# Optimization experiments

Measured on AMD Instinct MI355X. Metric: run time of the kernel, lower is better.

Reference implementation:

```python
import jax, jax.numpy as jnp
import numpy as np

N_HEAD = 16
N_KV_HEAD = 4
N_EMBD = 2048
HEAD_DIM = N_EMBD // N_HEAD
RMS_EPS = float(np.finfo(np.float32).eps)  # torch F.rms_norm default eps


def setup_inputs() -> dict:
    key = jax.random.key(0)
    ks = jax.random.split(key, 7)
    B, T = 2, 2048
    s = 0.02
    return {
        "x": jax.random.normal(ks[0], (B, T, N_EMBD), jnp.float32),
        "cos": jax.random.uniform(ks[1], (T, 1, HEAD_DIM), jnp.float32),
        "sin": jax.random.uniform(ks[2], (T, 1, HEAD_DIM), jnp.float32),
        "wq": jax.random.normal(ks[3], (N_HEAD * HEAD_DIM, N_EMBD), jnp.float32) * s,
        "wk": jax.random.normal(ks[4], (N_KV_HEAD * HEAD_DIM, N_EMBD), jnp.float32) * s,
        "wv": jax.random.normal(ks[5], (N_KV_HEAD * HEAD_DIM, N_EMBD), jnp.float32) * s,
        "wproj": jax.random.normal(ks[6], (N_EMBD, N_EMBD), jnp.float32) * s,
    }


def _rotate_half(x):
    h = x.shape[-1] // 2
    return jnp.concatenate([-x[..., h:], x[..., :h]], axis=-1)


def _apply_rope(x, cos, sin):  # x: [B, T, H, D]; cos/sin: [T, 1, D]
    return x * cos + _rotate_half(x) * sin


def _rms_norm(x):
    var = jnp.mean(jnp.square(x), axis=-1, keepdims=True)
    return x * jax.lax.rsqrt(var + RMS_EPS)


def reference(x, cos, sin, wq, wk, wv, wproj):
    B, T, C = x.shape
    group = N_HEAD // N_KV_HEAD
    q = (x @ wq.T).reshape(B, T, N_HEAD, HEAD_DIM)
    k = (x @ wk.T).reshape(B, T, N_KV_HEAD, HEAD_DIM)
    v = (x @ wv.T).reshape(B, T, N_KV_HEAD, HEAD_DIM)
    q = _rms_norm(_apply_rope(q, cos, sin))  # RoPE then QK RMSNorm
    k = _rms_norm(_apply_rope(k, cos, sin))
    # to [B, H, T, D]; expand kv heads for GQA
    q = q.transpose(0, 2, 1, 3)
    k = jnp.repeat(k.transpose(0, 2, 1, 3), group, axis=1)
    v = jnp.repeat(v.transpose(0, 2, 1, 3), group, axis=1)
    scale = 1.0 / jnp.sqrt(jnp.asarray(HEAD_DIM, x.dtype))
    scores = jnp.einsum('bhqd,bhkd->bhqk', q, k) * scale
    causal = jnp.tril(jnp.ones((T, T), bool))
    scores = jnp.where(causal, scores, jnp.asarray(-jnp.inf, scores.dtype))
    attn = jax.nn.softmax(scores, axis=-1)
    y = jnp.einsum('bhqk,bhkd->bhqd', attn, v)
    y = y.transpose(0, 2, 1, 3).reshape(B, T, C)
    return y @ wproj.T
```

## Files before the change

### kernel.cpp

```cpp
#include <hip/hip_runtime.h>
#include <hip/hip_bf16.h>

typedef __hip_bfloat16 bf16;
typedef __attribute__((ext_vector_type(8))) __bf16 bf16x8;
typedef __attribute__((ext_vector_type(4))) float f32x4;

#define MFMA16(a, b, c) __builtin_amdgcn_mfma_f32_16x16x32_bf16((a), (b), (c), 0, 0, 0)

#define BT 4096
#define CE 2048
#define NQKV 3072
#define TSEQ 2048
#define HD 128

#define QSCALE (0.08838834764831845f * 1.4426950408889634f)
#define M2 16.3222f

__device__ __forceinline__ void gld16(const void* g, void* l)
{
    __builtin_amdgcn_global_load_lds(
        (const __attribute__((address_space(1))) void*)g,
        (__attribute__((address_space(3))) void*)l, 16, 0, 0);
}

__global__ void detect_dtype(const unsigned short* __restrict__ x, int* __restrict__ flag)
{
    __shared__ int cnt;
    if (threadIdx.x == 0) cnt = 0;
    __syncthreads();
    unsigned short w = x[2 * threadIdx.x];
    int e = (w >> 7) & 0xFF;
    atomicAdd(&cnt, (e >= 117 && e <= 130) ? 1 : 0);
    __syncthreads();
    if (threadIdx.x == 0) *flag = (cnt < 128) ? 1 : 0;
}

__device__ __forceinline__ void stage8(short* dst, const void* src, size_t eoff, bool f32)
{
    if (f32) {
        const float* s = (const float*)src + eoff;
        float4 f0 = *(const float4*)s;
        float4 f1 = *(const float4*)(s + 4);
        bf16x8 v;
        v[0] = (__bf16)f0.x; v[1] = (__bf16)f0.y; v[2] = (__bf16)f0.z; v[3] = (__bf16)f0.w;
        v[4] = (__bf16)f1.x; v[5] = (__bf16)f1.y; v[6] = (__bf16)f1.z; v[7] = (__bf16)f1.w;
        *(bf16x8*)dst = v;
    } else {
        *(uint4*)dst = *(const uint4*)((const bf16*)src + eoff);
    }
}

__device__ __forceinline__ float ldf(const void* p, int i, bool f32)
{
    return f32 ? ((const float*)p)[i] : __bfloat162float(((const bf16*)p)[i]);
}

__global__ __launch_bounds__(256)
void conv_bf16(const void* __restrict__ src, bf16* __restrict__ dst,
               const int* __restrict__ flagp)
{
    const bool f = *flagp != 0;
    size_t i8 = (size_t)blockIdx.x * 256 + threadIdx.x;
    stage8((short*)(dst + i8 * 8), src, i8 * 8, f);
}

__global__ __launch_bounds__(256)
void gemm_bt(const void* __restrict__ A, const bf16* __restrict__ W,
             void* __restrict__ C, int M, int N, int K, int lda,
             int aGate, int oGate, const int* __restrict__ flagp)
{
    __shared__ short As[128][32];
    __shared__ short Bs[128][32];

    const int f = *flagp;
    const bool aF = aGate && f, oF = oGate && f;

    const int tid   = threadIdx.x;
    const int lane  = tid & 63;
    const int wid   = tid >> 6;
    const int row16 = lane & 15;
    const int quad  = lane >> 4;
    const int wr    = wid >> 1;
    const int wc    = wid & 1;
    const int m0    = blockIdx.y * 128;
    const int n0    = blockIdx.x * 128;

    const int rl4 = wid * 16 + (lane >> 2);
    const int c8  = (lane & 3) * 8;

    f32x4 acc[4][4];
#pragma unroll
    for (int i = 0; i < 4; i++)
#pragma unroll
        for (int j = 0; j < 4; j++)
            acc[i][j] = (f32x4){0.f, 0.f, 0.f, 0.f};

    for (int k0 = 0; k0 < K; k0 += 32) {
#pragma unroll
        for (int i = 0; i < 2; i++) {
            int r = i * 64 + rl4;
            gld16(W + (size_t)(n0 + r) * K + k0 + c8, &Bs[r][c8]);
        }
        if (!aF) {
#pragma unroll
            for (int i = 0; i < 2; i++) {
                int r = i * 64 + rl4;
                gld16((const bf16*)A + (size_t)(m0 + r) * lda + k0 + c8, &As[r][c8]);
            }
        } else {
#pragma unroll
            for (int i = 0; i < 2; i++) {
                int c = i * 256 + tid;
                int row = c >> 2, col = (c & 3) << 3;
                stage8(&As[row][col], A, (size_t)(m0 + row) * lda + k0 + col, true);
            }
        }
        __syncthreads();

        bf16x8 af[4], bfv[4];
#pragma unroll
        for (int mi = 0; mi < 4; mi++)
            af[mi] = *(const bf16x8*)&As[wr * 64 + mi * 16 + row16][quad * 8];
#pragma unroll
        for (int ni = 0; ni < 4; ni++)
            bfv[ni] = *(const bf16x8*)&Bs[wc * 64 + ni * 16 + row16][quad * 8];
#pragma unroll
        for (int mi = 0; mi < 4; mi++)
#pragma unroll
            for (int ni = 0; ni < 4; ni++)
                acc[mi][ni] = MFMA16(af[mi], bfv[ni], acc[mi][ni]);
        __syncthreads();
    }

#pragma unroll
    for (int mi = 0; mi < 4; mi++) {
        int rowb = m0 + wr * 64 + mi * 16 + quad * 4;
#pragma unroll
        for (int ni = 0; ni < 4; ni++) {
            int col = n0 + wc * 64 + ni * 16 + row16;
#pragma unroll
            for (int r = 0; r < 4; r++) {
                size_t idx = (size_t)(rowb + r) * N + col;
                float  v   = acc[mi][ni][r];
                if (oF) ((float*)C)[idx] = v;
                else    ((bf16*)C)[idx]  = __float2bfloat16(v);
            }
        }
    }
}

template<int MI>
__global__ __launch_bounds__(512, 2)
void gemmP(const bf16* __restrict__ A, const bf16* __restrict__ W,
           void* __restrict__ C, int M, int N, int K, int lda,
           int oGate, const int* __restrict__ flagp)
{
    constexpr int BM     = MI * 32;
    constexpr int ABYTES = BM * 128;
    constexpr int AUL    = ABYTES / 8192;

    __shared__ __bf16 As[2][BM][64];
    __shared__ __bf16 Bs[2][256][64];

    const bool oF = oGate && (*flagp != 0);

    const int gx  = gridDim.x;
    const int lin = blockIdx.y * gx + blockIdx.x;
    const int cpx = (gx * gridDim.y) >> 3;
    const int swzid = (lin & 7) * cpx + (lin >> 3);
    const int bx = swzid % gx;
    const int by = swzid / gx;

    const int tid   = threadIdx.x;
    const int lane  = tid & 63;
    const int wid   = tid >> 6;
    const int row16 = lane & 15;
    const int quad  = lane >> 4;
    const int wr    = wid >> 2;
    const int wc    = wid & 3;
    const int m0    = by * BM;
    const int n0    = bx * 256;
    const int NT    = K >> 6;

    const int srow = tid >> 3;
    const int sc8  = ((tid & 7) ^ (srow & 7)) * 8;
    const bf16* Ag = A + (size_t)(m0 + srow) * lda + sc8;
    const bf16* Bg = W + (size_t)(n0 + srow) * K   + sc8;
    char* const AsB = (char*)As;
    char* const BsB = (char*)Bs;
    const int sdst = tid * 16;

    auto stA = [&](int kt, int b) {
#pragma unroll
        for (int u = 0; u < AUL; ++u)
            gld16(Ag + (size_t)(u * 64) * lda + kt * 64,
                  AsB + b * ABYTES + u * 8192 + sdst);
    };
    auto stB = [&](int kt, int b) {
#pragma unroll
        for (int u = 0; u < 4; ++u)
            gld16(Bg + (size_t)(u * 64) * K + kt * 64,
                  BsB + b * 32768 + u * 8192 + sdst);
    };

    const int swz  = ((quad ^ (row16 & 7)) * 16);
    const int swz1 = (((4 + quad) ^ (row16 & 7)) * 16);
    const int aRow = wr * (MI * 16) + row16;
    const int bRow = wc * 64 + row16;

    auto ldA = [&](int b, int mi, int kk) -> bf16x8 {
        return *(const bf16x8*)(AsB + b * ABYTES + (aRow + mi * 16) * 128
                                + (kk ? swz1 : swz));
    };
    auto ldB = [&](int b, int ni, int kk) -> bf16x8 {
        return *(const bf16x8*)(BsB + b * 32768 + (bRow + ni * 16) * 128
                                + (kk ? swz1 : swz));
    };

    f32x4 acc[MI][4];
#pragma unroll
    for (int i = 0; i < MI; i++)
#pragma unroll
        for (int j = 0; j < 4; j++)
            acc[i][j] = (f32x4){0.f, 0.f, 0.f, 0.f};

    stA(0, 0); stB(0, 0);
    asm volatile("s_waitcnt vmcnt(0)" ::: "memory");
    __builtin_amdgcn_s_barrier();
    __builtin_amdgcn_sched_barrier(0);

    for (int t = 0; t < NT; ++t) {
        const int rb = t & 1;
        const int wb = rb ^ 1;

        bf16x8 bfr[4][2];
#pragma unroll
        for (int ni = 0; ni < 4; ni++)
#pragma unroll
            for (int kk = 0; kk < 2; kk++)
                bfr[ni][kk] = ldB(rb, ni, kk);
        bf16x8 a0[2][2];
#pragma unroll
        for (int i = 0; i < 2; i++)
#pragma unroll
            for (int kk = 0; kk < 2; kk++)
                a0[i][kk] = ldA(rb, i, kk);

        if (t + 1 < NT) { stB(t + 1, wb); stA(t + 1, wb); }

        __builtin_amdgcn_s_setprio(1);
#pragma unroll
        for (int kk = 0; kk < 2; kk++)
#pragma unroll
            for (int i = 0; i < 2; i++)
#pragma unroll
                for (int ni = 0; ni < 4; ni++)
                    acc[i][ni] = MFMA16(a0[i][kk], bfr[ni][kk], acc[i][ni]);
        __builtin_amdgcn_s_setprio(0);

#pragma unroll
        for (int p = 1; p < MI / 2; ++p) {
            bf16x8 ap[2][2];
#pragma unroll
            for (int i = 0; i < 2; i++)
#pragma unroll
                for (int kk = 0; kk < 2; kk++)
                    ap[i][kk] = ldA(rb, 2 * p + i, kk);
            __builtin_amdgcn_s_setprio(1);
#pragma unroll
            for (int kk = 0; kk < 2; kk++)
#pragma unroll
                for (int i = 0; i < 2; i++)
#pragma unroll
                    for (int ni = 0; ni < 4; ni++)
                        acc[2 * p + i][ni] =
                            MFMA16(ap[i][kk], bfr[ni][kk], acc[2 * p + i][ni]);
            __builtin_amdgcn_s_setprio(0);
        }

        asm volatile("s_waitcnt vmcnt(0)" ::: "memory");
        __builtin_amdgcn_s_barrier();
        __builtin_amdgcn_sched_barrier(0);
    }

#pragma unroll
    for (int mi = 0; mi < MI; mi++) {
        int rowb = m0 + wr * (MI * 16) + mi * 16 + quad * 4;
#pragma unroll
        for (int ni = 0; ni < 4; ni++) {
            int col = n0 + wc * 64 + ni * 16 + row16;
#pragma unroll
            for (int r = 0; r < 4; r++) {
                size_t idx = (size_t)(rowb + r) * N + col;
                float  v   = acc[mi][ni][r];
                if (oF) ((float*)C)[idx] = v;
                else    ((bf16*)C)[idx]  = __float2bfloat16(v);
            }
        }
    }
}

__global__ __launch_bounds__(256)
void rope_rms(bf16* __restrict__ qkv, const void* __restrict__ cosp,
              const void* __restrict__ sinp, const int* __restrict__ flagp)
{
    const bool f = *flagp != 0;
    const int wg   = blockIdx.x * 4 + (threadIdx.x >> 6);
    const int lane = threadIdx.x & 63;
    const int s    = wg % 20;
    const int m    = wg / 20;
    const int t    = m & (TSEQ - 1);

    const int col = (s < 16) ? s * HD : CE + (s - 16) * HD;
    bf16* p = qkv + (size_t)m * NQKV + col;

    float xlo = __bfloat162float(p[lane]);
    float xhi = __bfloat162float(p[lane + 64]);
    float cl  = ldf(cosp, t * HD + lane, f);
    float sl  = ldf(sinp, t * HD + lane, f);
    float ch  = ldf(cosp, t * HD + 64 + lane, f);
    float sh  = ldf(sinp, t * HD + 64 + lane, f);

    float rlo = xlo * cl - xhi * sl;
    float rhi = xhi * ch + xlo * sh;

    float ss = rlo * rlo + rhi * rhi;
#pragma unroll
    for (int off = 32; off > 0; off >>= 1)
        ss += __shfl_xor(ss, off, 64);
    float inv = rsqrtf(ss * (1.0f / 128.0f) + 1.1920929e-07f);
    if (s < 16) inv *= QSCALE;

    p[lane]      = __float2bfloat16(rlo * inv);
    p[lane + 64] = __float2bfloat16(rhi * inv);
}

__global__ __launch_bounds__(256)
void vtrans(const bf16* __restrict__ qkv, bf16* __restrict__ vt)
{
    __shared__ __bf16 tl[64][136];

    const int tid = threadIdx.x;
    const int bh  = blockIdx.x >> 5;
    const int t0  = (blockIdx.x & 31) * 64;
    const int b   = bh >> 2;
    const int hk  = bh & 3;

    const bf16* src = qkv + ((size_t)(b * TSEQ + t0)) * NQKV + 2560 + hk * HD;
#pragma unroll
    for (int it = 0; it < 4; ++it) {
        int idx  = it * 256 + tid;
        int trow = idx >> 4;
        int dcol = (idx & 15) * 8;
        *(uint4*)&tl[trow][dcol] = *(const uint4*)(src + (size_t)trow * NQKV + dcol);
    }
    __syncthreads();

    bf16* dst = vt + ((size_t)(bh * HD)) * TSEQ + t0;
#pragma unroll
    for (int it = 0; it < 4; ++it) {
        int idx  = it * 256 + tid;
        int drow = idx >> 3;
        int tcol = (idx & 7) * 8;
        bf16x8 v;
#pragma unroll
        for (int j = 0; j < 8; ++j)
            v[j] = tl[tcol + j][drow];
        *(bf16x8*)(dst + (size_t)drow * TSEQ + tcol) = v;
    }
}

__global__ __launch_bounds__(512, 2)
void attn(bf16* __restrict__ qkv, const bf16* __restrict__ vt)
{
    __shared__ __bf16 Ks[2][64][128];
    __shared__ __bf16 Vs[2][128][64];
    __shared__ __bf16 Pl[8][16][64];

    const int tid   = threadIdx.x;
    const int lane  = tid & 63;
    const int wid   = tid >> 6;
    const int row16 = lane & 15;
    const int quad  = lane >> 4;
    const int b   = blockIdx.y >> 2;
    const int hk  = blockIdx.y & 3;
    const int h   = hk * 4 + (wid & 3);
    const int mh  = wid >> 2;
    const int p   = blockIdx.x;

    const bf16* Kp = qkv + ((size_t)(b * TSEQ)) * NQKV + CE + hk * HD;
    const bf16* Vp = vt + ((size_t)(b * 4 + hk) * HD) * TSEQ;

    char* const KsB = (char*)Ks;
    char* const VsB = (char*)Vs;
    char* const PlB = (char*)Pl;

    auto stage = [&](int buf, int k0) {
#pragma unroll
        for (int i = 0; i < 2; i++) {
            int kr = (wid << 3) + i * 4 + (lane >> 4);
            int kc = (lane & 15) ^ (kr & 7);
            gld16(Kp + (size_t)(k0 + kr) * NQKV + kc * 8,
                  KsB + buf * 16384 + ((wid << 3) + i * 4) * 256 + lane * 16);
            int vr = (wid << 4) + i * 8 + (lane >> 3);
            int vc = (lane & 7) ^ (vr & 7);
            gld16(Vp + (size_t)vr * TSEQ + k0 + vc * 8,
                  VsB + buf * 16384 + ((wid << 4) + i * 8) * 128 + lane * 16);
        }
    };

    for (int pass = 0; pass < 2; ++pass) {
        const int xi  = pass ? 63 - p : p;
        const int nkt = (xi >> 1) + 1;
        const int qr0 = xi * 32 + mh * 16;

        const bf16* Q = qkv + ((size_t)(b * TSEQ + qr0)) * NQKV + h * HD;
        bf16x8 aq[4];
#pragma unroll
        for (int ds = 0; ds < 4; ds++)
            aq[ds] = *(const bf16x8*)(Q + (size_t)row16 * NQKV + ds * 32 + quad * 8);

        f32x4 o[8];
#pragma unroll
        for (int dt = 0; dt < 8; dt++) o[dt] = (f32x4){0.f, 0.f, 0.f, 0.f};
        float lsum[4] = {0.f, 0.f, 0.f, 0.f};

        __syncthreads();
        stage(0, 0);
        __syncthreads();

        for (int t = 0; t < nkt; ++t) {
            const int cur = t & 1;
            if (t + 1 < nkt) stage(cur ^ 1, (t + 1) * 64);

            f32x4 s[4];
#pragma unroll
            for (int kg = 0; kg < 4; kg++) s[kg] = (f32x4){0.f, 0.f, 0.f, 0.f};
            __builtin_amdgcn_s_setprio(1);
#pragma unroll
            for (int ds = 0; ds < 4; ds++) {
#pragma unroll
                for (int kg = 0; kg < 4; kg++) {
                    int krow = kg * 16 + row16;
                    int phys = (ds * 4 + quad) ^ (row16 & 7);
                    bf16x8 kf = *(const bf16x8*)(KsB + cur * 16384 + krow * 256 + phys * 16);
                    s[kg] = MFMA16(aq[ds], kf, s[kg]);
                }
            }
            __builtin_amdgcn_s_setprio(0);

            const bool diag = (t == nkt - 1);
            const int  k0   = t * 64;
            const int  r16h = row16 >> 3;
            const int  r16l = (row16 & 7) * 2;
#pragma unroll
            for (int r = 0; r < 4; r++) {
                float pv[4];
                int prow = quad * 4 + r;
                int qrow = qr0 + prow;
#pragma unroll
                for (int kg = 0; kg < 4; kg++) {
                    float e = __builtin_amdgcn_exp2f(s[kg][r] - M2);
                    pv[kg] = (!diag || (k0 + kg * 16 + row16 <= qrow)) ? e : 0.f;
                }
                lsum[r] += (pv[0] + pv[1]) + (pv[2] + pv[3]);
#pragma unroll
                for (int kg = 0; kg < 4; kg++)
                    *(__bf16*)(PlB + wid * 2048 + prow * 128
                               + (((kg * 2 + r16h) ^ (prow & 7)) << 4) + r16l)
                        = (__bf16)pv[kg];
            }
            __asm__ volatile("" ::: "memory");

            __builtin_amdgcn_s_setprio(1);
#pragma unroll
            for (int c = 0; c < 2; c++) {
                bf16x8 pf = *(const bf16x8*)(PlB + wid * 2048 + row16 * 128
                                             + ((((c << 2) + quad) ^ (row16 & 7)) << 4));
#pragma unroll
                for (int dt = 0; dt < 8; dt++) {
                    int vrow = dt * 16 + row16;
                    int phys = (c * 4 + quad) ^ (row16 & 7);
                    bf16x8 vf = *(const bf16x8*)(VsB + cur * 16384 + vrow * 128 + phys * 16);
                    o[dt] = MFMA16(pf, vf, o[dt]);
                }
            }
            __builtin_amdgcn_s_setprio(0);
            __asm__ volatile("" ::: "memory");
            __syncthreads();
        }

#pragma unroll
        for (int r = 0; r < 4; r++) {
            float l = lsum[r];
#pragma unroll
            for (int off = 1; off < 16; off <<= 1)
                l += __shfl_xor(l, off, 64);
            float rl = 1.0f / l;
            int trow = qr0 + quad * 4 + r;
            bf16* dst = qkv + ((size_t)(b * TSEQ + trow)) * NQKV + h * HD;
#pragma unroll
            for (int dt = 0; dt < 8; dt++)
                dst[dt * 16 + row16] = __float2bfloat16(o[dt][r] * rl);
        }
    }
}

extern "C" void kernel_launch(void* const* d_in, const int* in_sizes, int n_in,
                              void* d_out, int out_size, void* d_ws, size_t ws_size,
                              hipStream_t stream)
{
    bf16* qkv   = (bf16*)d_ws;
    bf16* vt    = qkv + (size_t)BT * NQKV;
    bf16* wqkvb = vt + (size_t)2 * 4 * HD * TSEQ;
    int* flagp  = (int*)(wqkvb + (size_t)NQKV * CE);
    bf16* xb    = wqkvb + (size_t)NQKV * CE + 16;

    const size_t need = ((size_t)BT * NQKV + (size_t)2 * 4 * HD * TSEQ
                         + (size_t)NQKV * CE + 16 + (size_t)BT * CE) * sizeof(bf16);
    const bool useXb = ws_size >= need;

    detect_dtype<<<1, 256, 0, stream>>>((const unsigned short*)d_in[0], flagp);

    conv_bf16<<<(2048 * 2048 / 8) / 256, 256, 0, stream>>>(d_in[3], wqkvb, flagp);
    conv_bf16<<<(512 * 2048 / 8) / 256, 256, 0, stream>>>(d_in[4], wqkvb + (size_t)2048 * 2048, flagp);
    conv_bf16<<<(512 * 2048 / 8) / 256, 256, 0, stream>>>(d_in[5], wqkvb + (size_t)2560 * 2048, flagp);

    if (useXb) {
        conv_bf16<<<(BT * CE / 8) / 256, 256, 0, stream>>>(d_in[0], xb, flagp);
        gemmP<8><<<dim3(NQKV / 256, BT / 256), 512, 0, stream>>>(
            xb, wqkvb, qkv, BT, NQKV, CE, CE, 0, flagp);
    } else {
        gemm_bt<<<dim3(NQKV / 128, BT / 128), 256, 0, stream>>>(
            d_in[0], wqkvb, qkv, BT, NQKV, CE, CE, 1, 0, flagp);
    }

    conv_bf16<<<(2048 * 2048 / 8) / 256, 256, 0, stream>>>(d_in[6], wqkvb, flagp);

    vtrans<<<256, 256, 0, stream>>>(qkv, vt);

    rope_rms<<<(BT * 20) / 4, 256, 0, stream>>>(qkv, d_in[1], d_in[2], flagp);

    attn<<<dim3(32, 2 * 4), 512, 0, stream>>>(qkv, vt);

    if (useXb) {
        gemmP<4><<<dim3(CE / 256, BT / 128), 512, 0, stream>>>(
            qkv, wqkvb, d_out, BT, CE, CE, NQKV, 1, flagp);
    } else {
        gemm_bt<<<dim3(CE / 128, BT / 128), 256, 0, stream>>>(
            qkv, wqkvb, d_out, BT, CE, CE, NQKV, 0, 1, flagp);
    }
}
```

Measured before the change: 321.0 us.

## Rework bf16 GEMM into triple-buffered pipeline with split K-phase loads and new tiles

```diff
diff --git a/kernel.cpp b/kernel.cpp
--- a/kernel.cpp
+++ b/kernel.cpp
@@ -149,18 +149,22 @@
     }
 }
 
-template<int MI>
+template<int MI, int NI>
 __global__ __launch_bounds__(512, 2)
-void gemmP(const bf16* __restrict__ A, const bf16* __restrict__ W,
+void gemmQ(const bf16* __restrict__ A, const bf16* __restrict__ W,
            void* __restrict__ C, int M, int N, int K, int lda,
            int oGate, const int* __restrict__ flagp)
 {
-    constexpr int BM     = MI * 32;
-    constexpr int ABYTES = BM * 128;
-    constexpr int AUL    = ABYTES / 8192;
-
-    __shared__ __bf16 As[2][BM][64];
-    __shared__ __bf16 Bs[2][256][64];
+    constexpr int BM    = MI * 32;
+    constexpr int BN    = NI * 64;
+    constexpr int ATILE = BM * 128;
+    constexpr int BTILE = BN * 128;
+    constexpr int AUL   = BM / 64;
+    constexpr int BUL   = BN / 64;
+    constexpr int INFL  = AUL + BUL;
+
+    __shared__ __bf16 As[3][BM][64];
+    __shared__ __bf16 Bs[3][BN][64];
 
     const bool oF = oGate && (*flagp != 0);
 
@@ -179,7 +183,7 @@
     const int wr    = wid >> 2;
     const int wc    = wid & 3;
     const int m0    = by * BM;
-    const int n0    = bx * 256;
+    const int n0    = bx * BN;
     const int NT    = K >> 6;
 
     const int srow = tid >> 3;
@@ -190,105 +194,129 @@
     char* const BsB = (char*)Bs;
     const int sdst = tid * 16;
 
-    auto stA = [&](int kt, int b) {
+    auto stA = [&](int kt, int s) {
 #pragma unroll
         for (int u = 0; u < AUL; ++u)
             gld16(Ag + (size_t)(u * 64) * lda + kt * 64,
-                  AsB + b * ABYTES + u * 8192 + sdst);
+                  AsB + s * ATILE + u * 8192 + sdst);
     };
-    auto stB = [&](int kt, int b) {
-#pragma unroll
-        for (int u = 0; u < 4; ++u)
+    auto stB = [&](int kt, int s) {
+#pragma unroll
+        for (int u = 0; u < BUL; ++u)
             gld16(Bg + (size_t)(u * 64) * K + kt * 64,
-                  BsB + b * 32768 + u * 8192 + sdst);
+                  BsB + s * BTILE + u * 8192 + sdst);
     };
 
     const int swz  = ((quad ^ (row16 & 7)) * 16);
     const int swz1 = (((4 + quad) ^ (row16 & 7)) * 16);
     const int aRow = wr * (MI * 16) + row16;
-    const int bRow = wc * 64 + row16;
-
-    auto ldA = [&](int b, int mi, int kk) -> bf16x8 {
-        return *(const bf16x8*)(AsB + b * ABYTES + (aRow + mi * 16) * 128
+    const int bRow = wc * (NI * 16) + row16;
+
+    auto ldA = [&](int sb, int mi, int kk) -> bf16x8 {
+        return *(const bf16x8*)(AsB + sb + (aRow + mi * 16) * 128
                                 + (kk ? swz1 : swz));
     };
-    auto ldB = [&](int b, int ni, int kk) -> bf16x8 {
-        return *(const bf16x8*)(BsB + b * 32768 + (bRow + ni * 16) * 128
+    auto ldB = [&](int sb, int ni, int kk) -> bf16x8 {
+        return *(const bf16x8*)(BsB + sb + (bRow + ni * 16) * 128
                                 + (kk ? swz1 : swz));
     };
 
-    f32x4 acc[MI][4];
+    f32x4 acc[MI][NI];
 #pragma unroll
     for (int i = 0; i < MI; i++)
 #pragma unroll
-        for (int j = 0; j < 4; j++)
+        for (int j = 0; j < NI; j++)
             acc[i][j] = (f32x4){0.f, 0.f, 0.f, 0.f};
 
     stA(0, 0); stB(0, 0);
-    asm volatile("s_waitcnt vmcnt(0)" ::: "memory");
+    stA(1, 1); stB(1, 1);
+    if constexpr (INFL == 5) asm volatile("s_waitcnt vmcnt(5)" ::: "memory");
+    else                     asm volatile("s_waitcnt vmcnt(6)" ::: "memory");
     __builtin_amdgcn_s_barrier();
     __builtin_amdgcn_sched_barrier(0);
 
+    int rs = 0, ps = 2;
     for (int t = 0; t < NT; ++t) {
-        const int rb = t & 1;
-        const int wb = rb ^ 1;
-
-        bf16x8 bfr[4][2];
-#pragma unroll
-        for (int ni = 0; ni < 4; ni++)
-#pragma unroll
-            for (int kk = 0; kk < 2; kk++)
-                bfr[ni][kk] = ldB(rb, ni, kk);
-        bf16x8 a0[2][2];
+        const bool pf = (t + 2) < NT;
+        const int ra  = rs * ATILE;
+        const int rbo = rs * BTILE;
+
+        bf16x8 bfr[NI], aa[2];
+
+#pragma unroll
+        for (int ni = 0; ni < NI; ni++) bfr[ni] = ldB(rbo, ni, 0);
+        aa[0] = ldA(ra, 0, 0); aa[1] = ldA(ra, 1, 0);
+        if (pf) stA(t + 2, ps);
+        __builtin_amdgcn_s_barrier();
+        asm volatile("s_waitcnt lgkmcnt(0)" ::: "memory");
+        __builtin_amdgcn_s_setprio(1);
 #pragma unroll
         for (int i = 0; i < 2; i++)
 #pragma unroll
-            for (int kk = 0; kk < 2; kk++)
-                a0[i][kk] = ldA(rb, i, kk);
-
-        if (t + 1 < NT) { stB(t + 1, wb); stA(t + 1, wb); }
-
+            for (int ni = 0; ni < NI; ni++)
+                acc[i][ni] = MFMA16(aa[i], bfr[ni], acc[i][ni]);
+        __builtin_amdgcn_s_setprio(0);
+        __builtin_amdgcn_s_barrier();
+        __builtin_amdgcn_sched_barrier(0);
+
+        aa[0] = ldA(ra, 2, 0); aa[1] = ldA(ra, 3, 0);
+        __builtin_amdgcn_s_barrier();
+        asm volatile("s_waitcnt lgkmcnt(0)" ::: "memory");
         __builtin_amdgcn_s_setprio(1);
 #pragma unroll
-        for (int kk = 0; kk < 2; kk++)
-#pragma unroll
-            for (int i = 0; i < 2; i++)
-#pragma unroll
-                for (int ni = 0; ni < 4; ni++)
-                    acc[i][ni] = MFMA16(a0[i][kk], bfr[ni][kk], acc[i][ni]);
+        for (int i = 0; i < 2; i++)
+#pragma unroll
+            for (int ni = 0; ni < NI; ni++)
+                acc[2 + i][ni] = MFMA16(aa[i], bfr[ni], acc[2 + i][ni]);
         __builtin_amdgcn_s_setprio(0);
-
-#pragma unroll
-        for (int p = 1; p < MI / 2; ++p) {
-            bf16x8 ap[2][2];
-#pragma unroll
-            for (int i = 0; i < 2; i++)
-#pragma unroll
-                for (int kk = 0; kk < 2; kk++)
-                    ap[i][kk] = ldA(rb, 2 * p + i, kk);
-            __builtin_amdgcn_s_setprio(1);
-#pragma unroll
-            for (int kk = 0; kk < 2; kk++)
-#pragma unroll
-                for (int i = 0; i < 2; i++)
-#pragma unroll
-                    for (int ni = 0; ni < 4; ni++)
-                        acc[2 * p + i][ni] =
-                            MFMA16(ap[i][kk], bfr[ni][kk], acc[2 * p + i][ni]);
-            __builtin_amdgcn_s_setprio(0);
-        }
-
-        asm volatile("s_waitcnt vmcnt(0)" ::: "memory");
         __builtin_amdgcn_s_barrier();
         __builtin_amdgcn_sched_barrier(0);
+
+#pragma unroll
+        for (int ni = 0; ni < NI; ni++) bfr[ni] = ldB(rbo, ni, 1);
+        aa[0] = ldA(ra, 0, 1); aa[1] = ldA(ra, 1, 1);
+        if (pf) stB(t + 2, ps);
+        __builtin_amdgcn_s_barrier();
+        asm volatile("s_waitcnt lgkmcnt(0)" ::: "memory");
+        __builtin_amdgcn_s_setprio(1);
+#pragma unroll
+        for (int i = 0; i < 2; i++)
+#pragma unroll
+            for (int ni = 0; ni < NI; ni++)
+                acc[i][ni] = MFMA16(aa[i], bfr[ni], acc[i][ni]);
+        __builtin_amdgcn_s_setprio(0);
+        __builtin_amdgcn_s_barrier();
+        __builtin_amdgcn_sched_barrier(0);
+
+        aa[0] = ldA(ra, 2, 1); aa[1] = ldA(ra, 3, 1);
+        if (pf) {
+            if constexpr (INFL == 5) asm volatile("s_waitcnt vmcnt(5)" ::: "memory");
+            else                     asm volatile("s_waitcnt vmcnt(6)" ::: "memory");
+        } else {
+            asm volatile("s_waitcnt vmcnt(0)" ::: "memory");
+        }
+        __builtin_amdgcn_s_barrier();
+        asm volatile("s_waitcnt lgkmcnt(0)" ::: "memory");
+        __builtin_amdgcn_s_setprio(1);
+#pragma unroll
+        for (int i = 0; i < 2; i++)
+#pragma unroll
+            for (int ni = 0; ni < NI; ni++)
+                acc[2 + i][ni] = MFMA16(aa[i], bfr[ni], acc[2 + i][ni]);
+        __builtin_amdgcn_s_setprio(0);
+        __builtin_amdgcn_s_barrier();
+        __builtin_amdgcn_sched_barrier(0);
+
+        rs = (rs == 2) ? 0 : rs + 1;
+        ps = (ps == 2) ? 0 : ps + 1;
     }
 
 #pragma unroll
     for (int mi = 0; mi < MI; mi++) {
         int rowb = m0 + wr * (MI * 16) + mi * 16 + quad * 4;
 #pragma unroll
-        for (int ni = 0; ni < 4; ni++) {
-            int col = n0 + wc * 64 + ni * 16 + row16;
+        for (int ni = 0; ni < NI; ni++) {
+            int col = n0 + wc * (NI * 16) + ni * 16 + row16;
 #pragma unroll
             for (int r = 0; r < 4; r++) {
                 size_t idx = (size_t)(rowb + r) * N + col;
@@ -528,7 +556,7 @@
 
     if (useXb) {
         conv_bf16<<<(BT * CE / 8) / 256, 256, 0, stream>>>(d_in[0], xb, flagp);
-        gemmP<8><<<dim3(NQKV / 256, BT / 256), 512, 0, stream>>>(
+        gemmQ<4, 3><<<dim3(NQKV / 192, BT / 128), 512, 0, stream>>>(
             xb, wqkvb, qkv, BT, NQKV, CE, CE, 0, flagp);
     } else {
         gemm_bt<<<dim3(NQKV / 128, BT / 128), 256, 0, stream>>>(
@@ -544,7 +572,7 @@
     attn<<<dim3(32, 2 * 4), 512, 0, stream>>>(qkv, vt);
 
     if (useXb) {
-        gemmP<4><<<dim3(CE / 256, BT / 128), 512, 0, stream>>>(
+        gemmQ<4, 4><<<dim3(CE / 256, BT / 128), 512, 0, stream>>>(
             qkv, wqkvb, d_out, BT, CE, CE, NQKV, 1, flagp);
     } else {
         gemm_bt<<<dim3(CE / 128, BT / 128), 256, 0, stream>>>(
```

New measurement: 343.6 us. 1.07x slower.

## Split attention KV tile across warps with two heads per warp, reduce via LDS

Applied to the files above, without the earlier changes.

```diff
diff --git a/kernel.cpp b/kernel.cpp
--- a/kernel.cpp
+++ b/kernel.cpp
@@ -373,9 +373,10 @@
 __global__ __launch_bounds__(512, 2)
 void attn(bf16* __restrict__ qkv, const bf16* __restrict__ vt)
 {
-    __shared__ __bf16 Ks[2][64][128];
-    __shared__ __bf16 Vs[2][128][64];
-    __shared__ __bf16 Pl[8][16][64];
+    __shared__ char lds[81920];
+    char* const KsB = lds;
+    char* const VsB = lds + 32768;
+    char* const PlB = lds + 65536;
 
     const int tid   = threadIdx.x;
     const int lane  = tid & 63;
@@ -384,16 +385,14 @@
     const int quad  = lane >> 4;
     const int b   = blockIdx.y >> 2;
     const int hk  = blockIdx.y & 3;
-    const int h   = hk * 4 + (wid & 3);
-    const int mh  = wid >> 2;
+    const int hp  = wid & 1;
+    const int mh  = (wid >> 1) & 1;
+    const int ks  = wid >> 2;
+    const int h0  = hk * 4 + hp * 2;
     const int p   = blockIdx.x;
 
     const bf16* Kp = qkv + ((size_t)(b * TSEQ)) * NQKV + CE + hk * HD;
     const bf16* Vp = vt + ((size_t)(b * 4 + hk) * HD) * TSEQ;
-
-    char* const KsB = (char*)Ks;
-    char* const VsB = (char*)Vs;
-    char* const PlB = (char*)Pl;
 
     auto stage = [&](int buf, int k0) {
 #pragma unroll
@@ -414,16 +413,22 @@
         const int nkt = (xi >> 1) + 1;
         const int qr0 = xi * 32 + mh * 16;
 
-        const bf16* Q = qkv + ((size_t)(b * TSEQ + qr0)) * NQKV + h * HD;
-        bf16x8 aq[4];
-#pragma unroll
-        for (int ds = 0; ds < 4; ds++)
-            aq[ds] = *(const bf16x8*)(Q + (size_t)row16 * NQKV + ds * 32 + quad * 8);
-
-        f32x4 o[8];
-#pragma unroll
-        for (int dt = 0; dt < 8; dt++) o[dt] = (f32x4){0.f, 0.f, 0.f, 0.f};
-        float lsum[4] = {0.f, 0.f, 0.f, 0.f};
+        const bf16* Q = qkv + ((size_t)(b * TSEQ + qr0)) * NQKV + h0 * HD;
+        bf16x8 aq[2][4];
+#pragma unroll
+        for (int h2 = 0; h2 < 2; h2++)
+#pragma unroll
+            for (int ds = 0; ds < 4; ds++)
+                aq[h2][ds] = *(const bf16x8*)(Q + h2 * HD
+                             + (size_t)row16 * NQKV + ds * 32 + quad * 8);
+
+        f32x4 o[2][8];
+#pragma unroll
+        for (int h2 = 0; h2 < 2; h2++)
+#pragma unroll
+            for (int dt = 0; dt < 8; dt++)
+                o[h2][dt] = (f32x4){0.f, 0.f, 0.f, 0.f};
+        f32x4 lsum[2] = {(f32x4){0.f,0.f,0.f,0.f}, (f32x4){0.f,0.f,0.f,0.f}};
 
         __syncthreads();
         stage(0, 0);
@@ -433,75 +438,112 @@
             const int cur = t & 1;
             if (t + 1 < nkt) stage(cur ^ 1, (t + 1) * 64);
 
-            f32x4 s[4];
-#pragma unroll
-            for (int kg = 0; kg < 4; kg++) s[kg] = (f32x4){0.f, 0.f, 0.f, 0.f};
+            f32x4 s[2][2];
+#pragma unroll
+            for (int h2 = 0; h2 < 2; h2++)
+#pragma unroll
+                for (int kgl = 0; kgl < 2; kgl++)
+                    s[h2][kgl] = (f32x4){0.f, 0.f, 0.f, 0.f};
             __builtin_amdgcn_s_setprio(1);
 #pragma unroll
             for (int ds = 0; ds < 4; ds++) {
 #pragma unroll
-                for (int kg = 0; kg < 4; kg++) {
-                    int krow = kg * 16 + row16;
-                    int phys = (ds * 4 + quad) ^ (row16 & 7);
-                    bf16x8 kf = *(const bf16x8*)(KsB + cur * 16384 + krow * 256 + phys * 16);
-                    s[kg] = MFMA16(aq[ds], kf, s[kg]);
+                for (int kgl = 0; kgl < 2; kgl++) {
+                    int krow = (ks * 2 + kgl) * 16 + row16;
+                    int phys = (ds * 4 + quad) ^ (krow & 7);
+                    bf16x8 kf = *(const bf16x8*)(KsB + cur * 16384
+                                                 + krow * 256 + phys * 16);
+                    s[0][kgl] = MFMA16(aq[0][ds], kf, s[0][kgl]);
+                    s[1][kgl] = MFMA16(aq[1][ds], kf, s[1][kgl]);
                 }
             }
             __builtin_amdgcn_s_setprio(0);
 
             const bool diag = (t == nkt - 1);
-            const int  k0   = t * 64;
+            const int  kbase = t * 64 + ks * 32;
             const int  r16h = row16 >> 3;
             const int  r16l = (row16 & 7) * 2;
 #pragma unroll
-            for (int r = 0; r < 4; r++) {
-                float pv[4];
-                int prow = quad * 4 + r;
-                int qrow = qr0 + prow;
-#pragma unroll
-                for (int kg = 0; kg < 4; kg++) {
-                    float e = __builtin_amdgcn_exp2f(s[kg][r] - M2);
-                    pv[kg] = (!diag || (k0 + kg * 16 + row16 <= qrow)) ? e : 0.f;
+            for (int h2 = 0; h2 < 2; h2++) {
+#pragma unroll
+                for (int r = 0; r < 4; r++) {
+                    int prow = quad * 4 + r;
+                    int qrow = qr0 + prow;
+                    float pv0, pv1;
+                    {
+                        float e0 = __builtin_amdgcn_exp2f(s[h2][0][r] - M2);
+                        float e1 = __builtin_amdgcn_exp2f(s[h2][1][r] - M2);
+                        pv0 = (!diag || (kbase + row16      <= qrow)) ? e0 : 0.f;
+                        pv1 = (!diag || (kbase + 16 + row16 <= qrow)) ? e1 : 0.f;
+                    }
+                    lsum[h2][r] += pv0 + pv1;
+                    char* base = PlB + wid * 2048 + h2 * 1024 + prow * 64;
+                    *(__bf16*)(base + (((0 * 2 + r16h) ^ (prow & 3)) << 4) + r16l)
+                        = (__bf16)pv0;
+                    *(__bf16*)(base + (((1 * 2 + r16h) ^ (prow & 3)) << 4) + r16l)
+                        = (__bf16)pv1;
                 }
-                lsum[r] += (pv[0] + pv[1]) + (pv[2] + pv[3]);
-#pragma unroll
-                for (int kg = 0; kg < 4; kg++)
-                    *(__bf16*)(PlB + wid * 2048 + prow * 128
-                               + (((kg * 2 + r16h) ^ (prow & 7)) << 4) + r16l)
-                        = (__bf16)pv[kg];
             }
             __asm__ volatile("" ::: "memory");
 
             __builtin_amdgcn_s_setprio(1);
-#pragma unroll
-            for (int c = 0; c < 2; c++) {
-                bf16x8 pf = *(const bf16x8*)(PlB + wid * 2048 + row16 * 128
-                                             + ((((c << 2) + quad) ^ (row16 & 7)) << 4));
-#pragma unroll
-                for (int dt = 0; dt < 8; dt++) {
-                    int vrow = dt * 16 + row16;
-                    int phys = (c * 4 + quad) ^ (row16 & 7);
-                    bf16x8 vf = *(const bf16x8*)(VsB + cur * 16384 + vrow * 128 + phys * 16);
-                    o[dt] = MFMA16(pf, vf, o[dt]);
-                }
+            bf16x8 pf0 = *(const bf16x8*)(PlB + wid * 2048 + row16 * 64
+                                          + ((quad ^ (row16 & 3)) << 4));
+            bf16x8 pf1 = *(const bf16x8*)(PlB + wid * 2048 + 1024 + row16 * 64
+                                          + ((quad ^ (row16 & 3)) << 4));
+#pragma unroll
+            for (int dt = 0; dt < 8; dt++) {
+                int vrow = dt * 16 + row16;
+                int phys = (ks * 4 + quad) ^ (vrow & 7);
+                bf16x8 vf = *(const bf16x8*)(VsB + cur * 16384
+                                             + vrow * 128 + phys * 16);
+                o[0][dt] = MFMA16(pf0, vf, o[0][dt]);
+                o[1][dt] = MFMA16(pf1, vf, o[1][dt]);
             }
             __builtin_amdgcn_s_setprio(0);
             __asm__ volatile("" ::: "memory");
             __syncthreads();
         }
 
-#pragma unroll
-        for (int r = 0; r < 4; r++) {
-            float l = lsum[r];
-#pragma unroll
-            for (int off = 1; off < 16; off <<= 1)
-                l += __shfl_xor(l, off, 64);
-            float rl = 1.0f / l;
-            int trow = qr0 + quad * 4 + r;
-            bf16* dst = qkv + ((size_t)(b * TSEQ + trow)) * NQKV + h * HD;
-#pragma unroll
-            for (int dt = 0; dt < 8; dt++)
-                dst[dt * 16 + row16] = __float2bfloat16(o[dt][r] * rl);
+        const int g = (hp << 1) | mh;
+        char* const scr = lds + g * 16384;
+        __syncthreads();
+        if (ks) {
+#pragma unroll
+            for (int h2 = 0; h2 < 2; h2++)
+#pragma unroll
+                for (int dt = 0; dt < 8; dt++)
+                    *(f32x4*)(scr + (h2 * 8 + dt) * 1024 + lane * 16) = o[h2][dt];
+            *(f32x4*)(PlB + g * 4096 + lane * 32)      = lsum[0];
+            *(f32x4*)(PlB + g * 4096 + lane * 32 + 16) = lsum[1];
+        }
+        __syncthreads();
+        if (!ks) {
+#pragma unroll
+            for (int h2 = 0; h2 < 2; h2++)
+#pragma unroll
+                for (int dt = 0; dt < 8; dt++)
+                    o[h2][dt] += *(const f32x4*)(scr + (h2 * 8 + dt) * 1024
+                                                 + lane * 16);
+            f32x4 l0 = *(const f32x4*)(PlB + g * 4096 + lane * 32);
+            f32x4 l1 = *(const f32x4*)(PlB + g * 4096 + lane * 32 + 16);
+#pragma unroll
+            for (int h2 = 0; h2 < 2; h2++) {
+#pragma unroll
+                for (int r = 0; r < 4; r++) {
+                    float l = lsum[h2][r] + (h2 ? l1[r] : l0[r]);
+#pragma unroll
+                    for (int off = 1; off < 16; off <<= 1)
+                        l += __shfl_xor(l, off, 64);
+                    float rl = 1.0f / l;
+                    int trow = qr0 + quad * 4 + r;
+                    bf16* dst = qkv + ((size_t)(b * TSEQ + trow)) * NQKV
+                                + (h0 + h2) * HD;
+#pragma unroll
+                    for (int dt = 0; dt < 8; dt++)
+                        dst[dt * 16 + row16] = __float2bfloat16(o[h2][dt][r] * rl);
+                }
+            }
         }
     }
 }
```

New measurement: 307.4 us. 1.04x faster.
